# Optimization experiments

Hardware: AMD Instinct MI355X
Metric: run time of the kernel (lower is better)

Reference implementation:

```python
import jax, jax.numpy as jnp
import numpy as np

N = 20000
NNBR = 64
MESH = (64, 64, 64)
ORDER = 4          # B-spline interpolation order
ALPHA = 0.35       # Ewald splitting parameter (1/Angstrom)
BOX = 73.68        # cubic box edge (Angstrom)
KE = 14.399645478425668  # Coulomb constant, eV*Angstrom/e^2


def _Mn(x, n):
    """Cardinal B-spline M_n(x), support [0, n]."""
    if n == 2:
        return jnp.maximum(0.0, 1.0 - jnp.abs(x - 1.0))
    return (x * _Mn(x, n - 1) + (n - x) * _Mn(x - 1.0, n - 1)) / (n - 1)


def _bspline_fac(K):
    """|b(m)|^-2 ... i.e. 1/|Euler spline denominator|^2 per mesh dim."""
    m = jnp.arange(K, dtype=jnp.float32)
    k = jnp.arange(ORDER - 1, dtype=jnp.float32)
    Mv = _Mn(k + 1.0, ORDER)                       # M_n(1..n-1)
    phase = 2.0 * jnp.pi * m[:, None] * k[None, :] / K
    dre = jnp.sum(Mv * jnp.cos(phase), axis=1)
    dim = jnp.sum(Mv * jnp.sin(phase), axis=1)
    return 1.0 / (dre * dre + dim * dim)


def _pme_energy(positions, charges, cell, nbr, shifts):
    n = positions.shape[0]
    # ---------------- real-space short-range sum ----------------
    i_idx = jnp.arange(n)[:, None]
    valid = (nbr >= 0) & ~((nbr == i_idx) & jnp.all(shifts == 0, axis=-1))
    j = jnp.where(nbr >= 0, nbr, 0)
    rvec = positions[j] + shifts.astype(positions.dtype) @ cell - positions[:, None, :]
    r2 = jnp.sum(rvec * rvec, axis=-1)
    r = jnp.sqrt(jnp.where(valid, r2, 1.0))
    qq = charges[:, None] * charges[j]
    e_real = 0.5 * jnp.sum(jnp.where(valid, qq * jax.scipy.special.erfc(ALPHA * r) / r, 0.0))
    # ---------------- B-spline charge spreading ----------------
    Kx, Ky, Kz = MESH
    frac = positions @ jnp.linalg.inv(cell)        # cell rows = lattice vectors
    u = frac * jnp.array(MESH, dtype=positions.dtype)
    base = jnp.floor(u)
    t = u - base                                   # in [0, 1)
    basei = base.astype(jnp.int32)
    offs = jnp.arange(ORDER)
    wx = _Mn(t[:, 0:1] + offs, ORDER)              # [N, ORDER]
    wy = _Mn(t[:, 1:2] + offs, ORDER)
    wz = _Mn(t[:, 2:3] + offs, ORDER)
    ix = (basei[:, 0:1] - offs) % Kx
    iy = (basei[:, 1:2] - offs) % Ky
    iz = (basei[:, 2:3] - offs) % Kz
    W = (charges[:, None] * wx)[:, :, None, None] * wy[:, None, :, None] * wz[:, None, None, :]
    IDX = (ix[:, :, None, None] * Ky + iy[:, None, :, None]) * Kz + iz[:, None, None, :]
    mesh = jnp.zeros(Kx * Ky * Kz, positions.dtype).at[IDX.reshape(-1)].add(W.reshape(-1)).reshape(MESH)
    # ---------------- reciprocal-space FFT convolution ----------------
    Q = jnp.fft.fftn(mesh)
    Brec = 2.0 * jnp.pi * jnp.linalg.inv(cell).T   # rows are reciprocal vectors
    mx = (jnp.fft.fftfreq(Kx) * Kx).astype(positions.dtype)
    my = (jnp.fft.fftfreq(Ky) * Ky).astype(positions.dtype)
    mz = (jnp.fft.fftfreq(Kz) * Kz).astype(positions.dtype)
    kvec = (mx[:, None, None, None] * Brec[0] + my[None, :, None, None] * Brec[1]
            + mz[None, None, :, None] * Brec[2])
    k2 = jnp.sum(kvec * kvec, axis=-1)
    a2 = ALPHA * ALPHA
    kern = jnp.where(k2 > 0, jnp.exp(-k2 / (4.0 * a2)) / jnp.where(k2 > 0, k2, 1.0), 0.0)
    C = _bspline_fac(Kx)[:, None, None] * _bspline_fac(Ky)[None, :, None] * _bspline_fac(Kz)[None, None, :]
    vol = jnp.abs(jnp.linalg.det(cell))
    e_rec = (2.0 * jnp.pi / vol) * jnp.sum(kern * C * (Q.real ** 2 + Q.imag ** 2))
    # ---------------- self + neutralizing background ----------------
    qtot = jnp.sum(charges)
    e_self = -(ALPHA / jnp.sqrt(jnp.pi)) * jnp.sum(charges * charges)
    e_bg = -(jnp.pi / (2.0 * a2 * vol)) * qtot * qtot
    return e_real + e_rec + e_self + e_bg


def setup_inputs() -> dict:
    key = jax.random.key(0)
    k1, k2, k3 = jax.random.split(key, 3)
    positions = jax.random.uniform(k1, (N, 3), jnp.float32) * BOX
    q = jax.random.normal(k2, (N,), jnp.float32)
    q = q - jnp.mean(q)  # neutral system
    cell = BOX * jnp.eye(3, dtype=jnp.float32)
    nbr = jax.random.randint(k3, (N, NNBR), 0, N, jnp.int32)
    shifts = jnp.zeros((N, NNBR, 3), jnp.int32)
    return {"positions": positions, "node_charges": q, "cell": cell,
            "neighbor_matrix": nbr, "neighbor_shifts": shifts}


def reference(positions, node_charges, cell, neighbor_matrix, neighbor_shifts):
    def e_strain(pos, q, c, eps):
        F = jnp.eye(3, dtype=pos.dtype) + eps
        return _pme_energy(pos @ F, q, c @ F, neighbor_matrix, neighbor_shifts)

    eps0 = jnp.zeros((3, 3), positions.dtype)
    e, (g_pos, g_eps) = jax.value_and_grad(e_strain, argnums=(0, 3))(
        positions, node_charges, cell, eps0)
    vol = jnp.abs(jnp.linalg.det(cell))
    energies = e.reshape(1) * KE
    forces = -g_pos * KE
    virial = -0.5 * (g_eps + g_eps.T) * KE
    stresses = (virial / vol)[None]
    return energies, forces, stresses
```

## Files before the change

### kernel.cpp

```cpp
#include <hip/hip_runtime.h>
#include <math.h>

#define NATOM 20000
#define NNBR  64
#define KM    64
#define KM3   (KM*KM*KM)
#define NPAIR (NATOM*NNBR)

#define ALPHA_C 0.35f
#define KE_C    14.399645478425668f
#define TWO_OVER_SQRTPI 1.1283791670955126f
#define TWOPI_F 6.2831853071795864f
#define PI_F    3.14159265358979f
#define RC2     661.2244898f

#define WS_RE    0
#define WS_IM    (KM3)
#define WS_MESH  (2*KM3)
#define WS_GJ    (3*KM3)
#define WS_PART  (3*KM3 + 3*NATOM)
#define WS_FI    (WS_PART + 1024)
#define WS_POSQ  (WS_FI + 3*NATOM)
#define WS_NBS   (WS_POSQ + 4*NATOM)
#define ZERO_LEN (KM3 + 3*NATOM + 1024)

__device__ __forceinline__ float M2f(float x){ return fmaxf(0.f, 1.f - fabsf(x - 1.f)); }
__device__ __forceinline__ float M3f(float x){ return (x*M2f(x) + (3.f-x)*M2f(x-1.f)) * 0.5f; }
__device__ __forceinline__ float M4f(float x){ return (x*M3f(x) + (4.f-x)*M3f(x-1.f)) * (1.f/3.f); }

__device__ __forceinline__ float wsum64(float v){
#pragma unroll
  for(int off=32; off>0; off>>=1) v += __shfl_xor(v, off, 64);
  return v;
}

__device__ __forceinline__ float hinv9(const float* __restrict__ cell, float* h){
  float m00=cell[0],m01=cell[1],m02=cell[2];
  float m10=cell[3],m11=cell[4],m12=cell[5];
  float m20=cell[6],m21=cell[7],m22=cell[8];
  float det = m00*(m11*m22-m12*m21) - m01*(m10*m22-m12*m20) + m02*(m10*m21-m11*m20);
  float id = 1.f/det;
  h[0]=(m11*m22-m12*m21)*id; h[1]=(m02*m21-m01*m22)*id; h[2]=(m01*m12-m02*m11)*id;
  h[3]=(m12*m20-m10*m22)*id; h[4]=(m00*m22-m02*m20)*id; h[5]=(m02*m10-m00*m12)*id;
  h[6]=(m10*m21-m11*m20)*id; h[7]=(m01*m20-m00*m21)*id; h[8]=(m00*m11-m01*m10)*id;
  return fabsf(det);
}

__device__ __forceinline__ void fill_tw(int t, float* twr, float* twi){
  if(t < 64){
    float ss, cc; sincosf((TWOPI_F/64.f)*(float)t, &ss, &cc);
    twr[t] = cc; twi[t] = -ss;
  }
}

__device__ __forceinline__ void fft64t(float& xr, float& xi, int lane,
                                       const float* __restrict__ twr,
                                       const float* __restrict__ twi, float sgn){
#pragma unroll
  for(int k=0;k<6;k++){
    int half = 32 >> k;
    float or_ = __shfl_xor(xr, half, 64);
    float oi_ = __shfl_xor(xi, half, 64);
    bool hi = (lane & half) != 0;
    float sr = hi ? (or_ - xr) : (xr + or_);
    float si = hi ? (oi_ - xi) : (xi + oi_);
    int e = (lane & (half-1)) << k;
    float wr2 = hi ? twr[e] : 1.f;
    float wi2 = hi ? sgn*twi[e] : 0.f;
    xr = sr*wr2 - si*wi2;
    xi = sr*wi2 + si*wr2;
  }
  int rev = __brev((unsigned)lane) >> 26;
  xr = __shfl(xr, rev, 64);
  xi = __shfl(xi, rev, 64);
}

__global__ __launch_bounds__(256) void init_kernel(
    const float* __restrict__ pos, const float* __restrict__ q,
    const int* __restrict__ nbr, const int* __restrict__ shifts,
    float* __restrict__ zbase, float4* __restrict__ posq, int* __restrict__ nbs){
  int t = blockIdx.x*256 + threadIdx.x;
  if(t < ZERO_LEN) zbase[t] = 0.f;
  if(t < NATOM)
    posq[t] = make_float4(pos[3*t], pos[3*t+1], pos[3*t+2], q[t]);
  if(t < NPAIR){
    int j = nbr[t];
    int sx=shifts[3*t], sy=shifts[3*t+1], sz=shifts[3*t+2];
    int v;
    if(j < 0) v = -1;
    else v = (j & 0x7FFF) | ((sx+8)&15)<<15 | ((sy+8)&15)<<19 | ((sz+8)&15)<<23;
    nbs[t] = v;
  }
}

__global__ __launch_bounds__(256) void real_kernel(
    const float4* __restrict__ posq, const int* __restrict__ nbs,
    const float* __restrict__ cell,
    float* __restrict__ fi, float* __restrict__ gj, float* __restrict__ part){
  int lane = threadIdx.x & 63;
  int wid  = blockIdx.x*4 + (threadIdx.x>>6);
  float c0=cell[0],c1=cell[1],c2=cell[2];
  float c3=cell[3],c4=cell[4],c5=cell[5];
  float c6=cell[6],c7=cell[7],c8=cell[8];
  float e=0.f, vxx=0.f,vyy=0.f,vzz=0.f,vxy=0.f,vxz=0.f,vyz=0.f;
#pragma unroll
  for(int it=0; it<4; ++it){
    int i = wid*4 + it;
    float4 pi4 = posq[i];
    int v = nbs[i*NNBR + lane];
    int j = v & 0x7FFF;
    int sx=((v>>15)&15)-8, sy=((v>>19)&15)-8, sz=((v>>23)&15)-8;
    bool self = (j==i) && (sx==0) && (sy==0) && (sz==0);
    float s=0.f, rx=0.f, ry=0.f, rz=0.f;
    if(v>=0 && !self){
      float4 pj = posq[j];
      rx = pj.x - pi4.x + sx*c0 + sy*c3 + sz*c6;
      ry = pj.y - pi4.y + sx*c1 + sy*c4 + sz*c7;
      rz = pj.z - pi4.z + sx*c2 + sy*c5 + sz*c8;
      float r2 = rx*rx + ry*ry + rz*rz;
      if(r2 > 0.f && r2 < RC2){
        float r = sqrtf(r2);
        float ar = ALPHA_C * r;
        float qq = pi4.w * pj.w;
        float ef = erfcf(ar);
        float ex = expf(-ar*ar);
        float ir = 1.f/r;
        e += 0.5f*qq*ef*ir;
        s  = 0.5f*qq*(ef + TWO_OVER_SQRTPI*ar*ex)*ir*ir*ir;
      }
    }
    float gx = s*rx, gy = s*ry, gz = s*rz;
    if(s != 0.f){
      unsafeAtomicAdd(&gj[3*j+0], -gx);
      unsafeAtomicAdd(&gj[3*j+1], -gy);
      unsafeAtomicAdd(&gj[3*j+2], -gz);
    }
    vxx -= s*rx*rx; vyy -= s*ry*ry; vzz -= s*rz*rz;
    vxy -= s*rx*ry; vxz -= s*rx*rz; vyz -= s*ry*rz;
    float tgx = wsum64(gx), tgy = wsum64(gy), tgz = wsum64(gz);
    if(lane==0){ fi[3*i]=tgx; fi[3*i+1]=tgy; fi[3*i+2]=tgz; }
  }
  e   = wsum64(e);
  vxx = wsum64(vxx); vyy = wsum64(vyy); vzz = wsum64(vzz);
  vxy = wsum64(vxy); vxz = wsum64(vxz); vyz = wsum64(vyz);
  if(lane==0){
    float* slot = part + (wid & 63)*16;
    unsafeAtomicAdd(&slot[0], e);
    unsafeAtomicAdd(&slot[1], vxx); unsafeAtomicAdd(&slot[2], vyy); unsafeAtomicAdd(&slot[3], vzz);
    unsafeAtomicAdd(&slot[4], vxy); unsafeAtomicAdd(&slot[5], vxz); unsafeAtomicAdd(&slot[6], vyz);
  }
}

__global__ __launch_bounds__(256) void spread_kernel(
    const float4* __restrict__ posq, const float* __restrict__ cell,
    float* __restrict__ mesh){
  int wid  = blockIdx.x*4 + (threadIdx.x>>6);
  int lane = threadIdx.x & 63;
  float h[9]; hinv9(cell, h);
  float4 pq = posq[wid];
  float u0=(pq.x*h[0]+pq.y*h[3]+pq.z*h[6])*(float)KM;
  float u1=(pq.x*h[1]+pq.y*h[4]+pq.z*h[7])*(float)KM;
  float u2=(pq.x*h[2]+pq.y*h[5]+pq.z*h[8])*(float)KM;
  float b0=floorf(u0), b1=floorf(u1), b2=floorf(u2);
  float t0=u0-b0, t1=u1-b1, t2=u2-b2;
  int i0=(int)b0, i1=(int)b1, i2=(int)b2;
  int a = lane>>4, b = (lane>>2)&3, c = lane&3;
  float w = pq.w * M4f(t0+(float)a) * M4f(t1+(float)b) * M4f(t2+(float)c);
  int ix=(i0-a+256)&63, iy=(i1-b+256)&63, iz=(i2-c+256)&63;
  unsafeAtomicAdd(&mesh[(ix*KM + iy)*KM + iz], w);
}

__global__ __launch_bounds__(256) void fftZF(const float* __restrict__ mesh,
                                             float* __restrict__ re, float* __restrict__ im){
  __shared__ float twr[64], twi[64];
  int t = threadIdx.x, lane = t&63;
  fill_tw(t, twr, twi);
  __syncthreads();
  int idx = blockIdx.x*256 + t;
  float xr = mesh[idx], xi = 0.f;
  fft64t(xr, xi, lane, twr, twi, 1.f);
  re[idx]=xr; im[idx]=xi;
}

__global__ __launch_bounds__(256) void fftZI(float* __restrict__ re, const float* __restrict__ im){
  __shared__ float twr[64], twi[64];
  int t = threadIdx.x, lane = t&63;
  fill_tw(t, twr, twi);
  __syncthreads();
  int idx = blockIdx.x*256 + t;
  float xr = re[idx], xi = im[idx];
  fft64t(xr, xi, lane, twr, twi, -1.f);
  re[idx]=xr;
}

__global__ __launch_bounds__(256) void fftY(float* __restrict__ re, float* __restrict__ im,
                                            float sgn){
  __shared__ float lr[64][17], li[64][17], twr[64], twi[64];
  int t = threadIdx.x, lane = t&63, w = t>>6;
  fill_tw(t, twr, twi);
  int x = blockIdx.x>>2, z0 = (blockIdx.x&3)*16;
  int off = x*4096 + z0;
#pragma unroll
  for(int k=0;k<4;k++){
    int e = k*256 + t; int y = e>>4, zz = e&15;
    lr[y][zz] = re[off + y*64 + zz];
    li[y][zz] = im[off + y*64 + zz];
  }
  __syncthreads();
#pragma unroll
  for(int qq=0; qq<4; qq++){
    int zz = w*4 + qq;
    float xr = lr[lane][zz], xi = li[lane][zz];
    fft64t(xr, xi, lane, twr, twi, sgn);
    lr[lane][zz] = xr; li[lane][zz] = xi;
  }
  __syncthreads();
#pragma unroll
  for(int k=0;k<4;k++){
    int e = k*256 + t; int y = e>>4, zz = e&15;
    re[off + y*64 + zz] = lr[y][zz];
    im[off + y*64 + zz] = li[y][zz];
  }
}

__global__ __launch_bounds__(256) void fftB(float* __restrict__ re, float* __restrict__ im,
                                            const float* __restrict__ cell,
                                            float* __restrict__ part){
  __shared__ float lr[64][17], li[64][17], cf[64], twr[64], twi[64];
  int t = threadIdx.x, lane = t&63, w = t>>6;
  int y = blockIdx.x>>2, z0 = (blockIdx.x&3)*16;
  float h[9]; hinv9(cell, h);
  fill_tw(t, twr, twi);
  if(t < 64){
    float p1 = TWOPI_F*(float)t/64.f;
    float s1,c1_,s2,c2_; sincosf(p1,&s1,&c1_); sincosf(2.f*p1,&s2,&c2_);
    float dre = (1.f/6.f) + (2.f/3.f)*c1_ + (1.f/6.f)*c2_;
    float dim = (2.f/3.f)*s1 + (1.f/6.f)*s2;
    cf[t] = 1.f/(dre*dre + dim*dim);
  }
  float* rp = re + y*64 + z0;
  float* ip = im + y*64 + z0;
#pragma unroll
  for(int k=0;k<4;k++){
    int e = k*256 + t; int xI = e>>4, zz = e&15;
    lr[xI][zz] = rp[xI*4096 + zz];
    li[xI][zz] = ip[xI*4096 + zz];
  }
  __syncthreads();
  const float inv4a2 = 1.f/(4.f*ALPHA_C*ALPHA_C);
  float my_f = (float)((y<32)? y : y-64);
  float sE=0.f, v0=0.f,v1=0.f,v2=0.f,v3=0.f,v4=0.f,v5=0.f;
#pragma unroll
  for(int qq=0; qq<4; qq++){
    int zz = w*4 + qq; int z = z0 + zz;
    float xr = lr[lane][zz], xi = li[lane][zz];
    fft64t(xr, xi, lane, twr, twi, 1.f);
    int mx = lane, mz = z;
    float fx = (float)((mx<32)? mx : mx-64);
    float fz = (float)((mz<32)? mz : mz-64);
    float kx = TWOPI_F*(fx*h[0] + my_f*h[1] + fz*h[2]);
    float ky = TWOPI_F*(fx*h[3] + my_f*h[4] + fz*h[5]);
    float kz = TWOPI_F*(fx*h[6] + my_f*h[7] + fz*h[8]);
    float k2 = kx*kx + ky*ky + kz*kz;
    float wk = 0.f;
    if(k2 > 0.f){
      float kern = expf(-k2*inv4a2)/k2;
      wk = kern * cf[mx]*cf[y]*cf[z];
      float q2 = xr*xr + xi*xi;
      sE += wk*q2;
      float fac = wk*q2*(inv4a2 + 1.f/k2)*2.f;
      v0 += fac*kx*kx; v1 += fac*ky*ky; v2 += fac*kz*kz;
      v3 += fac*kx*ky; v4 += fac*kx*kz; v5 += fac*ky*kz;
    }
    lr[lane][zz] = wk*xr; li[lane][zz] = wk*xi;
  }
  __syncthreads();
#pragma unroll
  for(int k=0;k<4;k++){
    int e = k*256 + t; int xI = e>>4, zz = e&15;
    rp[xI*4096 + zz] = lr[xI][zz];
    ip[xI*4096 + zz] = li[xI][zz];
  }
  sE = wsum64(sE);
  v0 = wsum64(v0); v1 = wsum64(v1); v2 = wsum64(v2);
  v3 = wsum64(v3); v4 = wsum64(v4); v5 = wsum64(v5);
  if(lane==0){
    float* slot = part + (((blockIdx.x<<2)|w)&63)*16;
    unsafeAtomicAdd(&slot[7],  sE);
    unsafeAtomicAdd(&slot[8],  v0); unsafeAtomicAdd(&slot[9],  v1);
    unsafeAtomicAdd(&slot[10], v2); unsafeAtomicAdd(&slot[11], v3);
    unsafeAtomicAdd(&slot[12], v4); unsafeAtomicAdd(&slot[13], v5);
  }
}

__global__ __launch_bounds__(256) void fftC(float* __restrict__ re, float* __restrict__ im){
  __shared__ float lr[64][17], li[64][17], twr[64], twi[64];
  int t = threadIdx.x, lane = t&63, w = t>>6;
  fill_tw(t, twr, twi);
  int y = blockIdx.x>>2, z0 = (blockIdx.x&3)*16;
  float* rp = re + y*64 + z0;
  float* ip = im + y*64 + z0;
#pragma unroll
  for(int k=0;k<4;k++){
    int e = k*256 + t; int xI = e>>4, zz = e&15;
    lr[xI][zz] = rp[xI*4096 + zz];
    li[xI][zz] = ip[xI*4096 + zz];
  }
  __syncthreads();
#pragma unroll
  for(int qq=0; qq<4; qq++){
    int zz = w*4 + qq;
    float xr = lr[lane][zz], xi = li[lane][zz];
    fft64t(xr, xi, lane, twr, twi, -1.f);
    lr[lane][zz] = xr; li[lane][zz] = xi;
  }
  __syncthreads();
#pragma unroll
  for(int k=0;k<4;k++){
    int e = k*256 + t; int xI = e>>4, zz = e&15;
    rp[xI*4096 + zz] = lr[xI][zz];
    ip[xI*4096 + zz] = li[xI][zz];
  }
}

__global__ __launch_bounds__(256) void gather_kernel(
    const float4* __restrict__ posq, const float* __restrict__ cell,
    const float* __restrict__ phi,
    const float* __restrict__ fi, const float* __restrict__ gj,
    const float* __restrict__ part, float* __restrict__ out){
  __shared__ float sa[256], sb[256], facc[16];
  int wid  = blockIdx.x*4 + (threadIdx.x>>6);
  int lane = threadIdx.x & 63;
  float h[9]; float V = hinv9(cell, h);
  float4 pq = posq[wid];
  float u0=(pq.x*h[0]+pq.y*h[3]+pq.z*h[6])*(float)KM;
  float u1=(pq.x*h[1]+pq.y*h[4]+pq.z*h[7])*(float)KM;
  float u2=(pq.x*h[2]+pq.y*h[5]+pq.z*h[8])*(float)KM;
  float b0=floorf(u0), b1=floorf(u1), b2=floorf(u2);
  float t0=u0-b0, t1=u1-b1, t2=u2-b2;
  int i0=(int)b0, i1=(int)b1, i2=(int)b2;
  int a = lane>>4, b = (lane>>2)&3, c = lane&3;
  float fa=(float)a, fb=(float)b, fc=(float)c;
  float wxa=M4f(t0+fa), wyb=M4f(t1+fb), wzc=M4f(t2+fc);
  float dxa=M3f(t0+fa)-M3f(t0+fa-1.f);
  float dyb=M3f(t1+fb)-M3f(t1+fb-1.f);
  float dzc=M3f(t2+fc)-M3f(t2+fc-1.f);
  int ix=(i0-a+256)&63, iy=(i1-b+256)&63, iz=(i2-c+256)&63;
  float p = phi[(ix*KM + iy)*KM + iz];
  float Sx = wsum64(p*dxa*wyb*wzc);
  float Sy = wsum64(p*wxa*dyb*wzc);
  float Sz = wsum64(p*wxa*wyb*dzc);
  if(lane==0){
    float scale = pq.w * (2.f*TWOPI_F/V) * (float)KM;
    float g0 = scale*(Sx*h[0] + Sy*h[1] + Sz*h[2]);
    float g1 = scale*(Sx*h[3] + Sy*h[4] + Sz*h[5]);
    float g2 = scale*(Sx*h[6] + Sy*h[7] + Sz*h[8]);
    out[1+3*wid+0] = -KE_C*(fi[3*wid+0] + gj[3*wid+0] + g0);
    out[1+3*wid+1] = -KE_C*(fi[3*wid+1] + gj[3*wid+1] + g1);
    out[1+3*wid+2] = -KE_C*(fi[3*wid+2] + gj[3*wid+2] + g2);
  }
  if(blockIdx.x==0){
    int t = threadIdx.x;
    float qa=0.f, qb=0.f;
    for(int i=t;i<NATOM;i+=256){ float qv=posq[i].w; qa+=qv; qb+=qv*qv; }
    sa[t]=qa; sb[t]=qb; __syncthreads();
    for(int off=128; off>0; off>>=1){
      if(t<off){ sa[t]+=sa[t+off]; sb[t]+=sb[t+off]; } __syncthreads();
    }
    if(t<14){ float s=0.f; for(int sl=0;sl<64;sl++) s+=part[sl*16+t]; facc[t]=s; }
    __syncthreads();
    if(t==0){
      float qtot = sa[0], sumq2 = sb[0];
      float a2 = ALPHA_C*ALPHA_C;
      float pref = TWOPI_F/V;
      float e_real = facc[0];
      float e_rec  = pref*facc[7];
      float e_self = -(ALPHA_C/sqrtf(PI_F))*sumq2;
      float e_bg   = -(PI_F/(2.f*a2*V))*qtot*qtot;
      out[0] = (e_real + e_rec + e_self + e_bg)*KE_C;
      float gxx = facc[1] + pref*facc[8]  - e_rec - e_bg;
      float gyy = facc[2] + pref*facc[9]  - e_rec - e_bg;
      float gzz = facc[3] + pref*facc[10] - e_rec - e_bg;
      float gxy = facc[4] + pref*facc[11];
      float gxz = facc[5] + pref*facc[12];
      float gyz = facc[6] + pref*facc[13];
      float cc = -KE_C/V;
      float* st = out + 1 + 3*NATOM;
      st[0]=cc*gxx; st[4]=cc*gyy; st[8]=cc*gzz;
      st[1]=cc*gxy; st[3]=cc*gxy;
      st[2]=cc*gxz; st[6]=cc*gxz;
      st[5]=cc*gyz; st[7]=cc*gyz;
    }
  }
}

extern "C" void kernel_launch(void* const* d_in, const int* in_sizes, int n_in,
                              void* d_out, int out_size, void* d_ws, size_t ws_size,
                              hipStream_t stream) {
  const float* pos  = (const float*)d_in[0];
  const float* q    = (const float*)d_in[1];
  const float* cell = (const float*)d_in[2];
  const int* nbr    = (const int*)d_in[3];
  const int* shifts = (const int*)d_in[4];
  float* out = (float*)d_out;
  float* ws  = (float*)d_ws;
  float*  bufRe = ws + WS_RE;
  float*  bufIm = ws + WS_IM;
  float*  mesh  = ws + WS_MESH;
  float*  gj    = ws + WS_GJ;
  float*  part  = ws + WS_PART;
  float*  fi    = ws + WS_FI;
  float4* posq  = (float4*)(ws + WS_POSQ);
  int*    nbs   = (int*)(ws + WS_NBS);

  init_kernel<<<(NPAIR+255)/256,256,0,stream>>>(pos, q, nbr, shifts, mesh, posq, nbs);
  real_kernel<<<1250,256,0,stream>>>(posq, nbs, cell, fi, gj, part);
  spread_kernel<<<5000,256,0,stream>>>(posq, cell, mesh);
  fftZF<<<1024,256,0,stream>>>(mesh, bufRe, bufIm);
  fftY <<< 256,256,0,stream>>>(bufRe, bufIm, 1.f);
  fftB <<< 256,256,0,stream>>>(bufRe, bufIm, cell, part);
  fftC <<< 256,256,0,stream>>>(bufRe, bufIm);
  fftY <<< 256,256,0,stream>>>(bufRe, bufIm, -1.f);
  fftZI<<<1024,256,0,stream>>>(bufRe, bufIm);
  gather_kernel<<<5000,256,0,stream>>>(posq, cell, bufRe, fi, gj, part, out);
}
```

Measured before the change: 189.1 us.

## Fuse inverse x-FFT into Green-function kernel and batch neighbor loads

The reciprocal-space multiply kernel now runs the inverse x-direction FFT on each pencil right after applying the Green-function weight, so the separate fftC launch and its full mesh read/write round trip are gone. The real-space kernel issues all four neighbor-index and position gathers up front, clamping the index so out-of-range lanes still load safely, which gives more memory-level parallelism in exchange for higher register use. Invalid pairs now compute a displacement that is masked out instead of skipping the load.

```diff
diff --git a/kernel.cpp b/kernel.cpp
--- a/kernel.cpp
+++ b/kernel.cpp
@@ -99,35 +99,40 @@
     float* __restrict__ fi, float* __restrict__ gj, float* __restrict__ part){
   int lane = threadIdx.x & 63;
   int wid  = blockIdx.x*4 + (threadIdx.x>>6);
+  int i0   = wid*4;
   float c0=cell[0],c1=cell[1],c2=cell[2];
   float c3=cell[3],c4=cell[4],c5=cell[5];
   float c6=cell[6],c7=cell[7],c8=cell[8];
+  int v[4]; int jj[4]; float4 pi[4], pj[4];
+#pragma unroll
+  for(int k=0;k<4;k++) v[k]  = nbs[(i0+k)*NNBR + lane];
+#pragma unroll
+  for(int k=0;k<4;k++) pi[k] = posq[i0+k];
+#pragma unroll
+  for(int k=0;k<4;k++) jj[k] = min(v[k] & 0x7FFF, NATOM-1);
+#pragma unroll
+  for(int k=0;k<4;k++) pj[k] = posq[jj[k]];
   float e=0.f, vxx=0.f,vyy=0.f,vzz=0.f,vxy=0.f,vxz=0.f,vyz=0.f;
 #pragma unroll
-  for(int it=0; it<4; ++it){
-    int i = wid*4 + it;
-    float4 pi4 = posq[i];
-    int v = nbs[i*NNBR + lane];
-    int j = v & 0x7FFF;
-    int sx=((v>>15)&15)-8, sy=((v>>19)&15)-8, sz=((v>>23)&15)-8;
-    bool self = (j==i) && (sx==0) && (sy==0) && (sz==0);
-    float s=0.f, rx=0.f, ry=0.f, rz=0.f;
-    if(v>=0 && !self){
-      float4 pj = posq[j];
-      rx = pj.x - pi4.x + sx*c0 + sy*c3 + sz*c6;
-      ry = pj.y - pi4.y + sx*c1 + sy*c4 + sz*c7;
-      rz = pj.z - pi4.z + sx*c2 + sy*c5 + sz*c8;
-      float r2 = rx*rx + ry*ry + rz*rz;
-      if(r2 > 0.f && r2 < RC2){
-        float r = sqrtf(r2);
-        float ar = ALPHA_C * r;
-        float qq = pi4.w * pj.w;
-        float ef = erfcf(ar);
-        float ex = expf(-ar*ar);
-        float ir = 1.f/r;
-        e += 0.5f*qq*ef*ir;
-        s  = 0.5f*qq*(ef + TWO_OVER_SQRTPI*ar*ex)*ir*ir*ir;
-      }
+  for(int k=0;k<4;k++){
+    int i = i0 + k;
+    int vv = v[k], j = jj[k];
+    int sx=((vv>>15)&15)-8, sy=((vv>>19)&15)-8, sz=((vv>>23)&15)-8;
+    bool valid = (vv>=0) && !((j==i) && (sx==0) && (sy==0) && (sz==0));
+    float rx = pj[k].x - pi[k].x + sx*c0 + sy*c3 + sz*c6;
+    float ry = pj[k].y - pi[k].y + sx*c1 + sy*c4 + sz*c7;
+    float rz = pj[k].z - pi[k].z + sx*c2 + sy*c5 + sz*c8;
+    float r2 = rx*rx + ry*ry + rz*rz;
+    float s = 0.f;
+    if(valid && r2 > 0.f && r2 < RC2){
+      float r = sqrtf(r2);
+      float ar = ALPHA_C * r;
+      float qq = pi[k].w * pj[k].w;
+      float ef = erfcf(ar);
+      float ex = expf(-ar*ar);
+      float ir = 1.f/r;
+      e += 0.5f*qq*ef*ir;
+      s  = 0.5f*qq*(ef + TWO_OVER_SQRTPI*ar*ex)*ir*ir*ir;
     }
     float gx = s*rx, gy = s*ry, gz = s*rz;
     if(s != 0.f){
@@ -223,9 +228,9 @@
   }
 }
 
-__global__ __launch_bounds__(256) void fftB(float* __restrict__ re, float* __restrict__ im,
-                                            const float* __restrict__ cell,
-                                            float* __restrict__ part){
+__global__ __launch_bounds__(256) void fftBC(float* __restrict__ re, float* __restrict__ im,
+                                             const float* __restrict__ cell,
+                                             float* __restrict__ part){
   __shared__ float lr[64][17], li[64][17], cf[64], twr[64], twi[64];
   int t = threadIdx.x, lane = t&63, w = t>>6;
   int y = blockIdx.x>>2, z0 = (blockIdx.x&3)*16;
@@ -272,7 +277,9 @@
       v0 += fac*kx*kx; v1 += fac*ky*ky; v2 += fac*kz*kz;
       v3 += fac*kx*ky; v4 += fac*kx*kz; v5 += fac*ky*kz;
     }
-    lr[lane][zz] = wk*xr; li[lane][zz] = wk*xi;
+    xr *= wk; xi *= wk;
+    fft64t(xr, xi, lane, twr, twi, -1.f);
+    lr[lane][zz] = xr; li[lane][zz] = xi;
   }
   __syncthreads();
 #pragma unroll
@@ -290,36 +297,6 @@
     unsafeAtomicAdd(&slot[8],  v0); unsafeAtomicAdd(&slot[9],  v1);
     unsafeAtomicAdd(&slot[10], v2); unsafeAtomicAdd(&slot[11], v3);
     unsafeAtomicAdd(&slot[12], v4); unsafeAtomicAdd(&slot[13], v5);
-  }
-}
-
-__global__ __launch_bounds__(256) void fftC(float* __restrict__ re, float* __restrict__ im){
-  __shared__ float lr[64][17], li[64][17], twr[64], twi[64];
-  int t = threadIdx.x, lane = t&63, w = t>>6;
-  fill_tw(t, twr, twi);
-  int y = blockIdx.x>>2, z0 = (blockIdx.x&3)*16;
-  float* rp = re + y*64 + z0;
-  float* ip = im + y*64 + z0;
-#pragma unroll
-  for(int k=0;k<4;k++){
-    int e = k*256 + t; int xI = e>>4, zz = e&15;
-    lr[xI][zz] = rp[xI*4096 + zz];
-    li[xI][zz] = ip[xI*4096 + zz];
-  }
-  __syncthreads();
-#pragma unroll
-  for(int qq=0; qq<4; qq++){
-    int zz = w*4 + qq;
-    float xr = lr[lane][zz], xi = li[lane][zz];
-    fft64t(xr, xi, lane, twr, twi, -1.f);
-    lr[lane][zz] = xr; li[lane][zz] = xi;
-  }
-  __syncthreads();
-#pragma unroll
-  for(int k=0;k<4;k++){
-    int e = k*256 + t; int xI = e>>4, zz = e&15;
-    rp[xI*4096 + zz] = lr[xI][zz];
-    ip[xI*4096 + zz] = li[xI][zz];
   }
 }
 
@@ -418,8 +395,7 @@
   spread_kernel<<<5000,256,0,stream>>>(posq, cell, mesh);
   fftZF<<<1024,256,0,stream>>>(mesh, bufRe, bufIm);
   fftY <<< 256,256,0,stream>>>(bufRe, bufIm, 1.f);
-  fftB <<< 256,256,0,stream>>>(bufRe, bufIm, cell, part);
-  fftC <<< 256,256,0,stream>>>(bufRe, bufIm);
+  fftBC<<< 256,256,0,stream>>>(bufRe, bufIm, cell, part);
   fftY <<< 256,256,0,stream>>>(bufRe, bufIm, -1.f);
   fftZI<<<1024,256,0,stream>>>(bufRe, bufIm);
   gather_kernel<<<5000,256,0,stream>>>(posq, cell, bufRe, fi, gj, part, out);
```

Measured after the change: 185.6 us. About the same (-1.9%).
